# Kernel tuning notes

Measured on AMD Instinct MI355X. Metric: run time of the kernel, lower is better.

## Reference

```python
import jax, jax.numpy as jnp
import numpy as np

DIM = 64
B_GRAPHS = 16
N_NODES = 4096
N_EDGES = 16384
SLOPE = 0.01  # PyTorch leaky_relu default negative slope


def lrelu(x):
    return jnp.where(x >= 0, x, SLOPE * x)


def setup_inputs() -> dict:
    key = jax.random.key(0)
    ks = jax.random.split(key, 16)
    d = DIM

    def rn(k, shape, scale=0.05):
        return jax.random.normal(k, shape, dtype=jnp.float32) * scale

    def z(*s):
        return jnp.zeros(s, jnp.float32)

    return {
        "x": jax.random.normal(ks[0], (N_NODES, 3), dtype=jnp.float32),
        "edge_attr": jax.random.normal(ks[1], (N_EDGES, 4), dtype=jnp.float32),
        "edge_index": jax.random.randint(ks[2], (2, N_EDGES), 0, N_NODES),
        "batch": jnp.sort(jax.random.randint(ks[3], (N_NODES,), 0, B_GRAPHS)),
        # lin0
        "W0": rn(ks[4], (3, d)), "b0": z(d),
        # edge MLP: Linear(4,d) -> LeakyReLU -> Linear(d, d*d)
        "We1": rn(ks[5], (4, d)), "be1": z(d),
        "We2": rn(ks[6], (d, d * d), 0.01), "be2": z(d * d),
        # NNConv root weight + bias
        "root": rn(ks[7], (d, d)), "conv_b": z(d),
        # GRU(d, d)  (PyTorch layout: [3d, in] / [3d, hid], gate order r,z,n)
        "Wih": rn(ks[8], (3 * d, d)), "Whh": rn(ks[9], (3 * d, d)),
        "bih": z(3 * d), "bhh": z(3 * d),
        # Set2Set LSTM(2d, d)  (gate order i,f,g,o)
        "lWih": rn(ks[10], (4 * d, 2 * d)), "lWhh": rn(ks[11], (4 * d, d)),
        "lbih": z(4 * d), "lbhh": z(4 * d),
        # lin_out: Linear(2d, 2)
        "Wout": rn(ks[12], (2 * d, 2)), "bout": z(2),
    }


def _forward(x, edge_attr, W0, b0, We1, be1, We2, be2, root, conv_b,
             Wih, Whh, bih, bhh, lWih, lWhh, lbih, lbhh, Wout, bout,
             edge_index, batch):
    d = DIM
    N = x.shape[0]
    E = edge_attr.shape[0]
    src, dst = edge_index[0], edge_index[1]  # messages flow src(j) -> dst(i)

    out = lrelu(x @ W0 + b0)  # [N, d]
    h = out                    # GRU hidden state (h = out.unsqueeze(0))

    # Edge-conditioned weights: constant across the 6 iterations, compute once.
    he = lrelu(edge_attr @ We1 + be1)          # [E, d]
    W_e = (he @ We2 + be2).reshape(E, d, d)    # [E, d, d]
    deg = jax.ops.segment_sum(jnp.ones((E,), jnp.float32), dst, num_segments=N)
    inv_deg = (1.0 / jnp.maximum(deg, 1.0))[:, None]  # mean aggr, clamp like PyG

    for _ in range(6):
        # NNConv: gather x_j, per-edge matmul, scatter-mean, plus root term
        msg = jnp.einsum('ed,edf->ef', out[src], W_e)            # [E, d]
        agg = jax.ops.segment_sum(msg, dst, num_segments=N) * inv_deg
        m = lrelu(agg + out @ root + conv_b)                     # [N, d]
        # GRU cell (single step, PyTorch gate order r, z, n)
        gi = m @ Wih.T + bih
        gh = h @ Whh.T + bhh
        i_r, i_z, i_n = jnp.split(gi, 3, axis=-1)
        h_r, h_z, h_n = jnp.split(gh, 3, axis=-1)
        r = jax.nn.sigmoid(i_r + h_r)
        zg = jax.nn.sigmoid(i_z + h_z)
        n = jnp.tanh(i_n + r * h_n)
        h = (1.0 - zg) * n + zg * h
        out = h

    # Set2Set pooling, processing_steps = 1
    Bg = B_GRAPHS
    q_star = jnp.zeros((Bg, 2 * d), jnp.float32)
    hl = jnp.zeros((Bg, d), jnp.float32)
    cl = jnp.zeros((Bg, d), jnp.float32)
    gates = q_star @ lWih.T + lbih + hl @ lWhh.T + lbhh
    gi_, gf_, gg_, go_ = jnp.split(gates, 4, axis=-1)
    cl = jax.nn.sigmoid(gf_) * cl + jax.nn.sigmoid(gi_) * jnp.tanh(gg_)
    q = jax.nn.sigmoid(go_) * jnp.tanh(cl)         # [Bg, d]
    e = jnp.sum(out * q[batch], axis=-1)           # [N]
    emax = jax.ops.segment_max(e, batch, num_segments=Bg)
    a = jnp.exp(e - emax[batch])
    asum = jax.ops.segment_sum(a, batch, num_segments=Bg)
    a = a / asum[batch]                            # per-graph softmax attention
    rpool = jax.ops.segment_sum(a[:, None] * out, batch, num_segments=Bg)
    q_star = jnp.concatenate([q, rpool], axis=-1)  # [Bg, 2d]

    return q_star @ Wout + bout                    # [Bg, 2]


def reference(x, edge_attr, edge_index, batch, W0, b0, We1, be1, We2, be2,
              root, conv_b, Wih, Whh, bih, bhh, lWih, lWhh, lbih, lbhh,
              Wout, bout):
    return _forward(x, edge_attr, W0, b0, We1, be1, We2, be2, root, conv_b,
                    Wih, Whh, bih, bhh, lWih, lWhh, lbih, lbhh, Wout, bout,
                    edge_index, batch)
```

## Files before the change

### kernel.cpp

```cpp
#include <hip/hip_runtime.h>
#include <cstddef>

#define NE 16384
#define NN 4096
#define BG 16
#define NT 16
#define ACH 8

__device__ __forceinline__ float lrelu(float v){ return v >= 0.f ? v : 0.01f*v; }
__device__ __forceinline__ float sigm(float v){ return 1.f/(1.f + expf(-v)); }

__global__ __launch_bounds__(256) void setup_kernel(
    const float* __restrict__ x, const float* __restrict__ ea,
    const int* __restrict__ ei,
    const float* __restrict__ W0, const float* __restrict__ b0,
    const float* __restrict__ We1, const float* __restrict__ be1,
    const float* __restrict__ Wih, const float* __restrict__ Whh,
    float* __restrict__ W8T,
    float* __restrict__ h, float* __restrict__ he,
    int* __restrict__ deg, int* __restrict__ cnt)
{
    int t = blockIdx.x*256 + threadIdx.x;
    {
        int e = t >> 6, f = t & 63;
        float v = be1[f];
        #pragma unroll
        for (int d = 0; d < 4; ++d) v += ea[e*4+d]*We1[d*64+f];
        he[t] = lrelu(v);
    }
    if (t < NN*64) {
        int n = t >> 6, f = t & 63;
        float v = b0[f];
        #pragma unroll
        for (int d = 0; d < 3; ++d) v += x[n*3+d]*W0[d*64+f];
        h[t] = lrelu(v);
    }
    if (t < 32768) {
        int k = t >> 9, g = (t >> 3) & 63, j = t & 7;
        float v = 0.f;
        if (j < 3)      v = Wih[(j*64+g)*64 + k];
        else if (j < 6) v = Whh[((j-3)*64+g)*64 + k];
        W8T[t] = v;
    }
    if (t < NE) {
        atomicAdd(&deg[ei[NE + t]], 1);
        atomicAdd(&cnt[ei[t]], 1);
    }
}

__global__ __launch_bounds__(256) void scan_kernel(const int* __restrict__ cnt,
                                                   int* __restrict__ offs)
{
    __shared__ int ps[256];
    int t = threadIdx.x;
    int base = t*16;
    int loc[16];
    int s = 0;
    #pragma unroll
    for (int i = 0; i < 16; ++i) { loc[i] = s; s += cnt[base+i]; }
    ps[t] = s; __syncthreads();
    for (int off = 1; off < 256; off <<= 1) {
        int v = 0;
        if (t >= off) v = ps[t-off];
        __syncthreads();
        if (t >= off) ps[t] += v;
        __syncthreads();
    }
    int pre = (t == 0) ? 0 : ps[t-1];
    #pragma unroll
    for (int i = 0; i < 16; ++i) offs[base+i] = pre + loc[i];
    if (t == 255) offs[NN] = pre + s;
}

__global__ __launch_bounds__(256) void scatter_kernel(
    const int* __restrict__ ei, const int* __restrict__ offs,
    int* __restrict__ cnt,
    int* __restrict__ srcs, int* __restrict__ dsts, int* __restrict__ perm)
{
    int e = blockIdx.x*256 + threadIdx.x;
    if (e >= NE) return;
    int s = ei[e], d = ei[NE + e];
    int old = atomicSub(&cnt[s], 1);
    int pos = offs[s] + old - 1;
    srcs[pos] = s; dsts[pos] = d; perm[pos] = e;
}

__global__ __launch_bounds__(256) void reorder_kernel(
    const float* __restrict__ he, const int* __restrict__ perm,
    float* __restrict__ he_srt)
{
    int t = blockIdx.x*256 + threadIdx.x;
    he_srt[t] = he[(size_t)perm[t>>6]*64 + (t & 63)];
}

__global__ __launch_bounds__(256) void inv_range_kernel(
    const int* __restrict__ deg, const int* __restrict__ batch,
    float* __restrict__ inv_deg, int* __restrict__ gstart, int* __restrict__ gend)
{
    int n = blockIdx.x*256 + threadIdx.x;
    if (n >= NN) return;
    inv_deg[n] = 1.f / fmaxf((float)deg[n], 1.f);
    int b  = batch[n];
    int bp = (n == 0)    ? -1 : batch[n-1];
    int bn = (n == NN-1) ? BG : batch[n+1];
    for (int g = bp+1; g <= b; ++g) gstart[g] = n;
    for (int g = b;   g <  bn; ++g) gend[g]   = n+1;
    if (n == 0)    for (int g = 0;   g < b;  ++g) gend[g]   = 0;
    if (n == NN-1) for (int g = b+1; g < BG; ++g) gstart[g] = NN;
}

__global__ __launch_bounds__(1024) void conv_kernel(
    const float* __restrict__ h, const float* __restrict__ We2,
    const float* __restrict__ be2, const float* __restrict__ he_srt,
    const int* __restrict__ offs, const int* __restrict__ srcs,
    const int* __restrict__ dsts, float* __restrict__ agg)
{
    __shared__ float hsT[64][NT];
    __shared__ float Tb [NT][64];
    __shared__ float Tc [2][ACH][NT][64];
    __shared__ float he_s[2][128][ACH];
    int t  = threadIdx.x;
    int n0 = blockIdx.x * NT;

    { int n = t >> 6, i = t & 63; hsT[i][n] = h[(size_t)(n0+n)*64 + i]; }
    int ebase = offs[n0];
    int ecnt  = offs[n0+NT] - ebase;
    int eend  = ebase + ecnt;
    __syncthreads();

    int aT = t >> 6;
    int nT = ((t >> 4) & 3) * 4;
    int fT = (t & 15) * 4;
    int ct   = t - 512;
    int slot = ct >> 4;
    int f4   = (ct & 15) * 4;
    int nl0=-1,dt0=0,nl1=-1,dt1=0,nl2=-1,dt2=0,nl3=-1,dt3=0;
    float4 m0={0,0,0,0},m1={0,0,0,0},m2={0,0,0,0},m3={0,0,0,0};
    if (t >= 512) {
        if (slot      < ecnt) { nl0 = srcs[ebase+slot]    - n0; dt0 = dsts[ebase+slot];    }
        if (slot + 32 < ecnt) { nl1 = srcs[ebase+slot+32] - n0; dt1 = dsts[ebase+slot+32]; }
        if (slot + 64 < ecnt) { nl2 = srcs[ebase+slot+64] - n0; dt2 = dsts[ebase+slot+64]; }
        if (slot + 96 < ecnt) { nl3 = srcs[ebase+slot+96] - n0; dt3 = dsts[ebase+slot+96]; }
    }

#define EDGE_ACC(mj, nlj, row, buf_) \
    if (nlj >= 0) { \
        float4 hA = *(const float4*)&he_s[buf_][row][0]; \
        float4 hB = *(const float4*)&he_s[buf_][row][4]; \
        float4 t0 = *(const float4*)&Tc[buf_][0][nlj][f4]; \
        float4 t1 = *(const float4*)&Tc[buf_][1][nlj][f4]; \
        float4 t2 = *(const float4*)&Tc[buf_][2][nlj][f4]; \
        float4 t3 = *(const float4*)&Tc[buf_][3][nlj][f4]; \
        float4 t4 = *(const float4*)&Tc[buf_][4][nlj][f4]; \
        float4 t5 = *(const float4*)&Tc[buf_][5][nlj][f4]; \
        float4 t6 = *(const float4*)&Tc[buf_][6][nlj][f4]; \
        float4 t7 = *(const float4*)&Tc[buf_][7][nlj][f4]; \
        mj.x += hA.x*t0.x+hA.y*t1.x+hA.z*t2.x+hA.w*t3.x+hB.x*t4.x+hB.y*t5.x+hB.z*t6.x+hB.w*t7.x; \
        mj.y += hA.x*t0.y+hA.y*t1.y+hA.z*t2.y+hA.w*t3.y+hB.x*t4.y+hB.y*t5.y+hB.z*t6.y+hB.w*t7.y; \
        mj.z += hA.x*t0.z+hA.y*t1.z+hA.z*t2.z+hA.w*t3.z+hB.x*t4.z+hB.y*t5.z+hB.z*t6.z+hB.w*t7.z; \
        mj.w += hA.x*t0.w+hA.y*t1.w+hA.z*t2.w+hA.w*t3.w+hB.x*t4.w+hB.y*t5.w+hB.z*t6.w+hB.w*t7.w; \
    }

#define CONSUME(cm) { \
    int buf_ = (cm) & 1; \
    EDGE_ACC(m0, nl0, (slot),      buf_) \
    EDGE_ACC(m1, nl1, (slot+32),   buf_) \
    EDGE_ACC(m2, nl2, (slot+64),   buf_) \
    EDGE_ACC(m3, nl3, (slot+96),   buf_) \
    for (int e = ebase + 128 + slot; e < eend; e += 32) { \
        int nl = srcs[e] - n0, dtv = dsts[e]; \
        const float* hep = he_srt + (size_t)e*64 + (cm)*ACH; \
        float4 pm = {0,0,0,0}; \
        _Pragma("unroll") \
        for (int a = 0; a < ACH; ++a) { \
            float hv = hep[a]; \
            float4 tv = *(const float4*)&Tc[buf_][a][nl][f4]; \
            pm.x += hv*tv.x; pm.y += hv*tv.y; pm.z += hv*tv.z; pm.w += hv*tv.w; \
        } \
        if ((cm) == 0) { \
            float4 b = *(const float4*)&Tb[nl][f4]; \
            pm.x += b.x; pm.y += b.y; pm.z += b.z; pm.w += b.w; \
        } \
        float* ap = agg + (size_t)dtv*64 + f4; \
        atomicAdd(ap+0, pm.x); atomicAdd(ap+1, pm.y); \
        atomicAdd(ap+2, pm.z); atomicAdd(ap+3, pm.w); \
    } \
}

    for (int c = 0; c < 8; ++c) {
        if (t < 512) {
            const float* Wp = We2 + (size_t)(c*ACH + aT)*4096 + fT;
            float4 A0={0,0,0,0},A1={0,0,0,0},A2={0,0,0,0},A3={0,0,0,0};
            #pragma unroll 8
            for (int i = 0; i < 64; ++i) {
                float4 w  = *(const float4*)(Wp + (size_t)i*64);
                float4 hv = *(const float4*)&hsT[i][nT];
                A0.x += hv.x*w.x; A0.y += hv.x*w.y; A0.z += hv.x*w.z; A0.w += hv.x*w.w;
                A1.x += hv.y*w.x; A1.y += hv.y*w.y; A1.z += hv.y*w.z; A1.w += hv.y*w.w;
                A2.x += hv.z*w.x; A2.y += hv.z*w.y; A2.z += hv.z*w.z; A2.w += hv.z*w.w;
                A3.x += hv.w*w.x; A3.y += hv.w*w.y; A3.z += hv.w*w.z; A3.w += hv.w*w.w;
            }
            int buf = c & 1;
            *(float4*)&Tc[buf][aT][nT+0][fT] = A0;
            *(float4*)&Tc[buf][aT][nT+1][fT] = A1;
            *(float4*)&Tc[buf][aT][nT+2][fT] = A2;
            *(float4*)&Tc[buf][aT][nT+3][fT] = A3;
            if (c == 0) {
                #pragma unroll
                for (int r = 0; r < 2; ++r) {
                    int idx = t + r*512;
                    int n = idx >> 6, f = idx & 63;
                    float acc = 0.f;
                    #pragma unroll 8
                    for (int i = 0; i < 64; ++i) acc += hsT[i][n]*be2[i*64+f];
                    Tb[n][f] = acc;
                }
            }
        } else {
            {
                int le = ct >> 2, a2 = (ct & 3) * 2;
                if (ebase + le < NE)
                    *(float2*)&he_s[c&1][le][a2] =
                        *(const float2*)&he_srt[(size_t)(ebase+le)*64 + c*ACH + a2];
            }
            if (c >= 1) CONSUME(c-1);
        }
        __syncthreads();
    }
    if (t >= 512) {
        CONSUME(7);
        if (nl0 >= 0) {
            float4 b = *(const float4*)&Tb[nl0][f4];
            float* ap = agg + (size_t)dt0*64 + f4;
            atomicAdd(ap+0, m0.x+b.x); atomicAdd(ap+1, m0.y+b.y);
            atomicAdd(ap+2, m0.z+b.z); atomicAdd(ap+3, m0.w+b.w);
        }
        if (nl1 >= 0) {
            float4 b = *(const float4*)&Tb[nl1][f4];
            float* ap = agg + (size_t)dt1*64 + f4;
            atomicAdd(ap+0, m1.x+b.x); atomicAdd(ap+1, m1.y+b.y);
            atomicAdd(ap+2, m1.z+b.z); atomicAdd(ap+3, m1.w+b.w);
        }
        if (nl2 >= 0) {
            float4 b = *(const float4*)&Tb[nl2][f4];
            float* ap = agg + (size_t)dt2*64 + f4;
            atomicAdd(ap+0, m2.x+b.x); atomicAdd(ap+1, m2.y+b.y);
            atomicAdd(ap+2, m2.z+b.z); atomicAdd(ap+3, m2.w+b.w);
        }
        if (nl3 >= 0) {
            float4 b = *(const float4*)&Tb[nl3][f4];
            float* ap = agg + (size_t)dt3*64 + f4;
            atomicAdd(ap+0, m3.x+b.x); atomicAdd(ap+1, m3.y+b.y);
            atomicAdd(ap+2, m3.z+b.z); atomicAdd(ap+3, m3.w+b.w);
        }
    }
#undef CONSUME
#undef EDGE_ACC
}

__global__ __launch_bounds__(512) void node_kernel(
    const float* __restrict__ W8T, const float* __restrict__ root,
    const float* __restrict__ conv_b, const float* __restrict__ inv_deg,
    const float* __restrict__ bih, const float* __restrict__ bhh,
    float* __restrict__ h, float* __restrict__ agg)
{
    __shared__ float hs[8][64];
    __shared__ float ms[8][64];
    int t = threadIdx.x;
    int n = t >> 6, g = t & 63;
    int gn = blockIdx.x*8 + n;
    hs[n][g] = h[(size_t)gn*64 + g];
    __syncthreads();
    {
        size_t ix = (size_t)gn*64 + g;
        float v = agg[ix]*inv_deg[gn] + conv_b[g];
        agg[ix] = 0.f;
        #pragma unroll 8
        for (int k = 0; k < 64; ++k) v += hs[n][k]*root[k*64 + g];
        ms[n][g] = lrelu(v);
    }
    __syncthreads();

    float ir=0.f, iz=0.f, in_=0.f, hr=0.f, hz=0.f, hn=0.f;
    const float* Wp = W8T + (size_t)g*8;
    #pragma unroll 8
    for (int k = 0; k < 64; ++k) {
        float am = ms[n][k], ah = hs[n][k];
        float4 w0 = *(const float4*)(Wp + (size_t)k*512);
        float4 w1 = *(const float4*)(Wp + (size_t)k*512 + 4);
        ir  += am*w0.x; iz += am*w0.y; in_ += am*w0.z;
        hr  += ah*w0.w; hz += ah*w1.x; hn  += ah*w1.y;
    }
    float r  = sigm(ir + bih[g]      + hr + bhh[g]);
    float z  = sigm(iz + bih[64+g]   + hz + bhh[64+g]);
    float nn = tanhf(in_ + bih[128+g] + r*(hn + bhh[128+g]));
    h[(size_t)gn*64 + g] = (1.f - z)*nn + z*hs[n][g];
}

__device__ __forceinline__ float q_val(const float* lbih, const float* lbhh, int g)
{
    float gi = lbih[g]     + lbhh[g];
    float gg = lbih[128+g] + lbhh[128+g];
    float go = lbih[192+g] + lbhh[192+g];
    return sigm(go)*tanhf(sigm(gi)*tanhf(gg));
}

__global__ __launch_bounds__(256) void e_kernel(
    const float* __restrict__ h, const float* __restrict__ lbih,
    const float* __restrict__ lbhh, float* __restrict__ e)
{
    __shared__ float qs[64];
    int t = threadIdx.x;
    if (t < 64) qs[t] = q_val(lbih, lbhh, t);
    __syncthreads();
    int w = t >> 6, f = t & 63;
    int n = blockIdx.x*4 + w;
    float p = h[(size_t)n*64 + f]*qs[f];
    #pragma unroll
    for (int off = 32; off; off >>= 1) p += __shfl_xor(p, off);
    if (f == 0) e[n] = p;
}

__global__ __launch_bounds__(1024) void pool_kernel(
    const float* __restrict__ h, float* __restrict__ e,
    const int* __restrict__ gstart, const int* __restrict__ gend,
    const float* __restrict__ lbih, const float* __restrict__ lbhh,
    const float* __restrict__ Wout, const float* __restrict__ bout,
    float* __restrict__ out)
{
    __shared__ float red[1024];
    __shared__ float rp[64];
    __shared__ float sval;
    int g = blockIdx.x, t = threadIdx.x;
    int s = gstart[g], en = gend[g];

    float mx = -1e30f;
    for (int n = s+t; n < en; n += 1024) mx = fmaxf(mx, e[n]);
    red[t] = mx; __syncthreads();
    for (int st = 512; st; st >>= 1) { if (t < st) red[t] = fmaxf(red[t], red[t+st]); __syncthreads(); }
    if (t == 0) sval = red[0];
    __syncthreads();
    float lmx = sval;
    __syncthreads();

    float sm = 0.f;
    for (int n = s+t; n < en; n += 1024) { float a = expf(e[n]-lmx); e[n] = a; sm += a; }
    red[t] = sm; __syncthreads();
    for (int st = 512; st; st >>= 1) { if (t < st) red[t] += red[t+st]; __syncthreads(); }
    if (t == 0) sval = (red[0] > 0.f) ? 1.f/red[0] : 0.f;
    __syncthreads();
    float inv_asum = sval;
    __syncthreads();

    int w = t >> 6, f = t & 63;
    float racc = 0.f;
    for (int n = s+w; n < en; n += 16) racc += e[n]*h[(size_t)n*64 + f];
    red[t] = racc; __syncthreads();
    if (w == 0) {
        float a = 0.f;
        #pragma unroll
        for (int i = 0; i < 16; ++i) a += red[i*64 + f];
        rp[f] = a*inv_asum;
    }
    __syncthreads();

    if (t < 64) {
        float qv = q_val(lbih, lbhh, t);
        float p0 = qv*Wout[t*2]   + rp[t]*Wout[(64+t)*2];
        float p1 = qv*Wout[t*2+1] + rp[t]*Wout[(64+t)*2+1];
        #pragma unroll
        for (int off = 32; off; off >>= 1) { p0 += __shfl_xor(p0, off); p1 += __shfl_xor(p1, off); }
        if (t == 0) { out[g*2] = p0 + bout[0]; out[g*2+1] = p1 + bout[1]; }
    }
}

extern "C" void kernel_launch(void* const* d_in, const int* in_sizes, int n_in,
                              void* d_out, int out_size, void* d_ws, size_t ws_size,
                              hipStream_t stream)
{
    const float* x      = (const float*)d_in[0];
    const float* ea     = (const float*)d_in[1];
    const int*   ei     = (const int*)  d_in[2];
    const int*   batch  = (const int*)  d_in[3];
    const float* W0     = (const float*)d_in[4];
    const float* b0     = (const float*)d_in[5];
    const float* We1    = (const float*)d_in[6];
    const float* be1    = (const float*)d_in[7];
    const float* We2    = (const float*)d_in[8];
    const float* be2    = (const float*)d_in[9];
    const float* root   = (const float*)d_in[10];
    const float* conv_b = (const float*)d_in[11];
    const float* Wih    = (const float*)d_in[12];
    const float* Whh    = (const float*)d_in[13];
    const float* bih    = (const float*)d_in[14];
    const float* bhh    = (const float*)d_in[15];
    const float* lbih   = (const float*)d_in[18];
    const float* lbhh   = (const float*)d_in[19];
    const float* Wout   = (const float*)d_in[20];
    const float* bout   = (const float*)d_in[21];
    float* out = (float*)d_out;

    float* W = (float*)d_ws;
    size_t off = 0;
    float* h       = W + off; off += (size_t)NN*64;
    float* he      = W + off; off += (size_t)NE*64;
    float* he_srt  = W + off; off += (size_t)NE*64;
    float* agg     = W + off; off += (size_t)NN*64;
    float* W8T     = W + off; off += 32768;
    float* inv_deg = W + off; off += NN;
    float* e       = W + off; off += NN;
    int*   deg     = (int*)(W + off); off += NN;
    int*   cnt     = (int*)(W + off); off += NN;
    int*   offs    = (int*)(W + off); off += NN+1;
    int*   srcs    = (int*)(W + off); off += NE;
    int*   dsts    = (int*)(W + off); off += NE;
    int*   perm    = (int*)(W + off); off += NE;
    int*   gstart  = (int*)(W + off); off += BG;
    int*   gend    = (int*)(W + off); off += BG;

    hipMemsetAsync(deg, 0, 2*NN*sizeof(int), stream);
    hipMemsetAsync(agg, 0, (size_t)NN*64*sizeof(float), stream);
    setup_kernel<<<4096, 256, 0, stream>>>(x, ea, ei, W0, b0, We1, be1, Wih, Whh,
                                           W8T, h, he, deg, cnt);
    scan_kernel<<<1, 256, 0, stream>>>(cnt, offs);
    scatter_kernel<<<64, 256, 0, stream>>>(ei, offs, cnt, srcs, dsts, perm);
    reorder_kernel<<<4096, 256, 0, stream>>>(he, perm, he_srt);
    inv_range_kernel<<<16, 256, 0, stream>>>(deg, batch, inv_deg, gstart, gend);

    for (int it = 0; it < 6; ++it) {
        conv_kernel<<<NN/NT, 1024, 0, stream>>>(h, We2, be2, he_srt,
                                                offs, srcs, dsts, agg);
        node_kernel<<<NN/8, 512, 0, stream>>>(W8T, root, conv_b,
                                              inv_deg, bih, bhh, h, agg);
    }

    e_kernel<<<NN/4, 256, 0, stream>>>(h, lbih, lbhh, e);
    pool_kernel<<<BG, 1024, 0, stream>>>(h, e, gstart, gend, lbih, lbhh, Wout, bout, out);
}
```

Baseline: 558.0 us.

## Retile conv kernel to 2x8 register blocks, prefetch We2, move bias GEMV to consumer threads

The producer half of the conv kernel now computes a 2-node by 8-feature tile per thread instead of 4x4, stores h in a paired layout, and software-prefetches the next We2 rows to hide global load latency. The per-node bias term (h·be2) moves from producer threads at chunk 0 to the otherwise idle consumer threads. Consumer threads each handle 8 features and two resident edges instead of four features and four edges. The aim is fewer LDS reads per FMA and a shorter critical path for the producers, at the cost of higher register pressure and different atomic and edge-loop strides.

Result: slower. 830.6 us (+48.9%).

```diff
diff --git a/kernel.cpp b/kernel.cpp
--- a/kernel.cpp
+++ b/kernel.cpp
@@ -9,6 +9,9 @@
 
 __device__ __forceinline__ float lrelu(float v){ return v >= 0.f ? v : 0.01f*v; }
 __device__ __forceinline__ float sigm(float v){ return 1.f/(1.f + expf(-v)); }
+__device__ __forceinline__ void fma4(float4& a, float s, const float4& w){
+    a.x += s*w.x; a.y += s*w.y; a.z += s*w.z; a.w += s*w.w;
+}
 
 __global__ __launch_bounds__(256) void setup_kernel(
     const float* __restrict__ x, const float* __restrict__ ea,
@@ -115,107 +118,111 @@
     const int* __restrict__ offs, const int* __restrict__ srcs,
     const int* __restrict__ dsts, float* __restrict__ agg)
 {
-    __shared__ float hsT[64][NT];
+    __shared__ float hs2[32][16][2];
     __shared__ float Tb [NT][64];
     __shared__ float Tc [2][ACH][NT][64];
     __shared__ float he_s[2][128][ACH];
     int t  = threadIdx.x;
     int n0 = blockIdx.x * NT;
 
-    { int n = t >> 6, i = t & 63; hsT[i][n] = h[(size_t)(n0+n)*64 + i]; }
+    if (t < 512) {
+        int n = t & 15, r2 = t >> 4;
+        *(float2*)&hs2[r2][n][0] = *(const float2*)&h[(size_t)(n0+n)*64 + r2*2];
+    }
     int ebase = offs[n0];
     int ecnt  = offs[n0+NT] - ebase;
     int eend  = ebase + ecnt;
     __syncthreads();
 
-    int aT = t >> 6;
-    int nT = ((t >> 4) & 3) * 4;
-    int fT = (t & 15) * 4;
+    int aT  = t >> 6;
+    int nA  = ((t >> 3) & 7)*2;
+    int fT8 = (t & 7) * 8;
     int ct   = t - 512;
-    int slot = ct >> 4;
-    int f4   = (ct & 15) * 4;
-    int nl0=-1,dt0=0,nl1=-1,dt1=0,nl2=-1,dt2=0,nl3=-1,dt3=0;
-    float4 m0={0,0,0,0},m1={0,0,0,0},m2={0,0,0,0},m3={0,0,0,0};
+    int slot = ct >> 3;
+    int cf8  = (ct & 7) * 8;
+    int nl0=-1, dt0=0, nl1=-1, dt1=0;
+    float4 m0a={0,0,0,0}, m0b={0,0,0,0}, m1a={0,0,0,0}, m1b={0,0,0,0};
     if (t >= 512) {
         if (slot      < ecnt) { nl0 = srcs[ebase+slot]    - n0; dt0 = dsts[ebase+slot];    }
-        if (slot + 32 < ecnt) { nl1 = srcs[ebase+slot+32] - n0; dt1 = dsts[ebase+slot+32]; }
-        if (slot + 64 < ecnt) { nl2 = srcs[ebase+slot+64] - n0; dt2 = dsts[ebase+slot+64]; }
-        if (slot + 96 < ecnt) { nl3 = srcs[ebase+slot+96] - n0; dt3 = dsts[ebase+slot+96]; }
-    }
-
-#define EDGE_ACC(mj, nlj, row, buf_) \
+        if (slot + 64 < ecnt) { nl1 = srcs[ebase+slot+64] - n0; dt1 = dsts[ebase+slot+64]; }
+    }
+
+#define EDGE_ACC(mA, mB, nlj, row, buf_) \
     if (nlj >= 0) { \
         float4 hA = *(const float4*)&he_s[buf_][row][0]; \
         float4 hB = *(const float4*)&he_s[buf_][row][4]; \
-        float4 t0 = *(const float4*)&Tc[buf_][0][nlj][f4]; \
-        float4 t1 = *(const float4*)&Tc[buf_][1][nlj][f4]; \
-        float4 t2 = *(const float4*)&Tc[buf_][2][nlj][f4]; \
-        float4 t3 = *(const float4*)&Tc[buf_][3][nlj][f4]; \
-        float4 t4 = *(const float4*)&Tc[buf_][4][nlj][f4]; \
-        float4 t5 = *(const float4*)&Tc[buf_][5][nlj][f4]; \
-        float4 t6 = *(const float4*)&Tc[buf_][6][nlj][f4]; \
-        float4 t7 = *(const float4*)&Tc[buf_][7][nlj][f4]; \
-        mj.x += hA.x*t0.x+hA.y*t1.x+hA.z*t2.x+hA.w*t3.x+hB.x*t4.x+hB.y*t5.x+hB.z*t6.x+hB.w*t7.x; \
-        mj.y += hA.x*t0.y+hA.y*t1.y+hA.z*t2.y+hA.w*t3.y+hB.x*t4.y+hB.y*t5.y+hB.z*t6.y+hB.w*t7.y; \
-        mj.z += hA.x*t0.z+hA.y*t1.z+hA.z*t2.z+hA.w*t3.z+hB.x*t4.z+hB.y*t5.z+hB.z*t6.z+hB.w*t7.z; \
-        mj.w += hA.x*t0.w+hA.y*t1.w+hA.z*t2.w+hA.w*t3.w+hB.x*t4.w+hB.y*t5.w+hB.z*t6.w+hB.w*t7.w; \
+        float he8[8] = {hA.x,hA.y,hA.z,hA.w,hB.x,hB.y,hB.z,hB.w}; \
+        _Pragma("unroll") \
+        for (int a_ = 0; a_ < 8; ++a_) { \
+            float4 tA = *(const float4*)&Tc[buf_][a_][nlj][cf8]; \
+            float4 tB = *(const float4*)&Tc[buf_][a_][nlj][cf8+4]; \
+            fma4(mA, he8[a_], tA); \
+            fma4(mB, he8[a_], tB); \
+        } \
     }
 
 #define CONSUME(cm) { \
     int buf_ = (cm) & 1; \
-    EDGE_ACC(m0, nl0, (slot),      buf_) \
-    EDGE_ACC(m1, nl1, (slot+32),   buf_) \
-    EDGE_ACC(m2, nl2, (slot+64),   buf_) \
-    EDGE_ACC(m3, nl3, (slot+96),   buf_) \
-    for (int e = ebase + 128 + slot; e < eend; e += 32) { \
+    EDGE_ACC(m0a, m0b, nl0, slot,      buf_) \
+    EDGE_ACC(m1a, m1b, nl1, slot+64,   buf_) \
+    for (int e = ebase + 128 + slot; e < eend; e += 64) { \
         int nl = srcs[e] - n0, dtv = dsts[e]; \
         const float* hep = he_srt + (size_t)e*64 + (cm)*ACH; \
-        float4 pm = {0,0,0,0}; \
+        float4 pa = {0,0,0,0}, pb = {0,0,0,0}; \
         _Pragma("unroll") \
-        for (int a = 0; a < ACH; ++a) { \
-            float hv = hep[a]; \
-            float4 tv = *(const float4*)&Tc[buf_][a][nl][f4]; \
-            pm.x += hv*tv.x; pm.y += hv*tv.y; pm.z += hv*tv.z; pm.w += hv*tv.w; \
+        for (int a_ = 0; a_ < 8; ++a_) { \
+            float hv = hep[a_]; \
+            float4 tA = *(const float4*)&Tc[buf_][a_][nl][cf8]; \
+            float4 tB = *(const float4*)&Tc[buf_][a_][nl][cf8+4]; \
+            fma4(pa, hv, tA); \
+            fma4(pb, hv, tB); \
         } \
         if ((cm) == 0) { \
-            float4 b = *(const float4*)&Tb[nl][f4]; \
-            pm.x += b.x; pm.y += b.y; pm.z += b.z; pm.w += b.w; \
+            float4 bA = *(const float4*)&Tb[nl][cf8]; \
+            float4 bB = *(const float4*)&Tb[nl][cf8+4]; \
+            pa.x += bA.x; pa.y += bA.y; pa.z += bA.z; pa.w += bA.w; \
+            pb.x += bB.x; pb.y += bB.y; pb.z += bB.z; pb.w += bB.w; \
         } \
-        float* ap = agg + (size_t)dtv*64 + f4; \
-        atomicAdd(ap+0, pm.x); atomicAdd(ap+1, pm.y); \
-        atomicAdd(ap+2, pm.z); atomicAdd(ap+3, pm.w); \
+        float* ap = agg + (size_t)dtv*64 + cf8; \
+        atomicAdd(ap+0, pa.x); atomicAdd(ap+1, pa.y); \
+        atomicAdd(ap+2, pa.z); atomicAdd(ap+3, pa.w); \
+        atomicAdd(ap+4, pb.x); atomicAdd(ap+5, pb.y); \
+        atomicAdd(ap+6, pb.z); atomicAdd(ap+7, pb.w); \
     } \
 }
 
     for (int c = 0; c < 8; ++c) {
         if (t < 512) {
-            const float* Wp = We2 + (size_t)(c*ACH + aT)*4096 + fT;
-            float4 A0={0,0,0,0},A1={0,0,0,0},A2={0,0,0,0},A3={0,0,0,0};
-            #pragma unroll 8
-            for (int i = 0; i < 64; ++i) {
-                float4 w  = *(const float4*)(Wp + (size_t)i*64);
-                float4 hv = *(const float4*)&hsT[i][nT];
-                A0.x += hv.x*w.x; A0.y += hv.x*w.y; A0.z += hv.x*w.z; A0.w += hv.x*w.w;
-                A1.x += hv.y*w.x; A1.y += hv.y*w.y; A1.z += hv.y*w.z; A1.w += hv.y*w.w;
-                A2.x += hv.z*w.x; A2.y += hv.z*w.y; A2.z += hv.z*w.z; A2.w += hv.z*w.w;
-                A3.x += hv.w*w.x; A3.y += hv.w*w.y; A3.z += hv.w*w.z; A3.w += hv.w*w.w;
+            const float* Wp = We2 + (size_t)(c*ACH + aT)*4096 + fT8;
+            float4 a00={0,0,0,0}, a01={0,0,0,0}, a10={0,0,0,0}, a11={0,0,0,0};
+            float4 hv  = *(const float4*)&hs2[0][nA][0];
+            float4 wA0 = *(const float4*)(Wp);
+            float4 wA1 = *(const float4*)(Wp + 4);
+            float4 wB0 = *(const float4*)(Wp + 64);
+            float4 wB1 = *(const float4*)(Wp + 68);
+            #pragma unroll
+            for (int r2 = 0; r2 < 32; ++r2) {
+                float4 hvn={0,0,0,0}, wA0n={0,0,0,0}, wA1n={0,0,0,0},
+                       wB0n={0,0,0,0}, wB1n={0,0,0,0};
+                if (r2 < 31) {
+                    const float* Wn = Wp + (size_t)(r2+1)*128;
+                    hvn  = *(const float4*)&hs2[r2+1][nA][0];
+                    wA0n = *(const float4*)(Wn);
+                    wA1n = *(const float4*)(Wn + 4);
+                    wB0n = *(const float4*)(Wn + 64);
+                    wB1n = *(const float4*)(Wn + 68);
+                }
+                fma4(a00, hv.x, wA0); fma4(a01, hv.x, wA1);
+                fma4(a10, hv.z, wA0); fma4(a11, hv.z, wA1);
+                fma4(a00, hv.y, wB0); fma4(a01, hv.y, wB1);
+                fma4(a10, hv.w, wB0); fma4(a11, hv.w, wB1);
+                hv = hvn; wA0 = wA0n; wA1 = wA1n; wB0 = wB0n; wB1 = wB1n;
             }
             int buf = c & 1;
-            *(float4*)&Tc[buf][aT][nT+0][fT] = A0;
-            *(float4*)&Tc[buf][aT][nT+1][fT] = A1;
-            *(float4*)&Tc[buf][aT][nT+2][fT] = A2;
-            *(float4*)&Tc[buf][aT][nT+3][fT] = A3;
-            if (c == 0) {
-                #pragma unroll
-                for (int r = 0; r < 2; ++r) {
-                    int idx = t + r*512;
-                    int n = idx >> 6, f = idx & 63;
-                    float acc = 0.f;
-                    #pragma unroll 8
-                    for (int i = 0; i < 64; ++i) acc += hsT[i][n]*be2[i*64+f];
-                    Tb[n][f] = acc;
-                }
-            }
+            *(float4*)&Tc[buf][aT][nA  ][fT8]   = a00;
+            *(float4*)&Tc[buf][aT][nA  ][fT8+4] = a01;
+            *(float4*)&Tc[buf][aT][nA+1][fT8]   = a10;
+            *(float4*)&Tc[buf][aT][nA+1][fT8+4] = a11;
         } else {
             {
                 int le = ct >> 2, a2 = (ct & 3) * 2;
@@ -223,35 +230,44 @@
                     *(float2*)&he_s[c&1][le][a2] =
                         *(const float2*)&he_srt[(size_t)(ebase+le)*64 + c*ACH + a2];
             }
-            if (c >= 1) CONSUME(c-1);
+            if (c == 0) {
+                int n = ct >> 5, fp = (ct & 31) * 2;
+                float t0 = 0.f, t1 = 0.f;
+                #pragma unroll 8
+                for (int r2 = 0; r2 < 32; ++r2) {
+                    float2 hv2 = *(const float2*)&hs2[r2][n][0];
+                    float2 bA  = *(const float2*)&be2[(size_t)(r2*2)*64 + fp];
+                    float2 bB  = *(const float2*)&be2[(size_t)(r2*2+1)*64 + fp];
+                    t0 += hv2.x*bA.x + hv2.y*bB.x;
+                    t1 += hv2.x*bA.y + hv2.y*bB.y;
+                }
+                Tb[n][fp]   = t0;
+                Tb[n][fp+1] = t1;
+            } else {
+                CONSUME(c-1);
+            }
         }
         __syncthreads();
     }
     if (t >= 512) {
         CONSUME(7);
         if (nl0 >= 0) {
-            float4 b = *(const float4*)&Tb[nl0][f4];
-            float* ap = agg + (size_t)dt0*64 + f4;
-            atomicAdd(ap+0, m0.x+b.x); atomicAdd(ap+1, m0.y+b.y);
-            atomicAdd(ap+2, m0.z+b.z); atomicAdd(ap+3, m0.w+b.w);
+            float4 bA = *(const float4*)&Tb[nl0][cf8];
+            float4 bB = *(const float4*)&Tb[nl0][cf8+4];
+            float* ap = agg + (size_t)dt0*64 + cf8;
+            atomicAdd(ap+0, m0a.x+bA.x); atomicAdd(ap+1, m0a.y+bA.y);
+            atomicAdd(ap+2, m0a.z+bA.z); atomicAdd(ap+3, m0a.w+bA.w);
+            atomicAdd(ap+4, m0b.x+bB.x); atomicAdd(ap+5, m0b.y+bB.y);
+            atomicAdd(ap+6, m0b.z+bB.z); atomicAdd(ap+7, m0b.w+bB.w);
         }
         if (nl1 >= 0) {
-            float4 b = *(const float4*)&Tb[nl1][f4];
-            float* ap = agg + (size_t)dt1*64 + f4;
-            atomicAdd(ap+0, m1.x+b.x); atomicAdd(ap+1, m1.y+b.y);
-            atomicAdd(ap+2, m1.z+b.z); atomicAdd(ap+3, m1.w+b.w);
-        }
-        if (nl2 >= 0) {
-            float4 b = *(const float4*)&Tb[nl2][f4];
-            float* ap = agg + (size_t)dt2*64 + f4;
-            atomicAdd(ap+0, m2.x+b.x); atomicAdd(ap+1, m2.y+b.y);
-            atomicAdd(ap+2, m2.z+b.z); atomicAdd(ap+3, m2.w+b.w);
-        }
-        if (nl3 >= 0) {
-            float4 b = *(const float4*)&Tb[nl3][f4];
-            float* ap = agg + (size_t)dt3*64 + f4;
-            atomicAdd(ap+0, m3.x+b.x); atomicAdd(ap+1, m3.y+b.y);
-            atomicAdd(ap+2, m3.z+b.z); atomicAdd(ap+3, m3.w+b.w);
+            float4 bA = *(const float4*)&Tb[nl1][cf8];
+            float4 bB = *(const float4*)&Tb[nl1][cf8+4];
+            float* ap = agg + (size_t)dt1*64 + cf8;
+            atomicAdd(ap+0, m1a.x+bA.x); atomicAdd(ap+1, m1a.y+bA.y);
+            atomicAdd(ap+2, m1a.z+bA.z); atomicAdd(ap+3, m1a.w+bA.w);
+            atomicAdd(ap+4, m1b.x+bB.x); atomicAdd(ap+5, m1b.y+bB.y);
+            atomicAdd(ap+6, m1b.z+bB.z); atomicAdd(ap+7, m1b.w+bB.w);
         }
     }
 #undef CONSUME
```

## Remap conv GEMM threads to node-rows and move bias product to consumer warps

Applied to the files above, without the earlier changes.

Each producer thread in the per-chunk h·We2 product now owns one node row and 16 contiguous output columns, keeping 32 h values in registers and streaming four float4 weight loads per input row. The h tile and Tc buffers are padded to 68 columns to reduce LDS bank conflicts. The c==0 bias projection Tb moves from the producer threads to the otherwise idle consumer threads, balancing work in the first iteration. This raises register pressure and changes global access patterns for We2, which could affect occupancy.

Result: slower. 1.833 ms (+228.5%).

```diff
diff --git a/kernel.cpp b/kernel.cpp
--- a/kernel.cpp
+++ b/kernel.cpp
@@ -9,6 +9,9 @@
 
 __device__ __forceinline__ float lrelu(float v){ return v >= 0.f ? v : 0.01f*v; }
 __device__ __forceinline__ float sigm(float v){ return 1.f/(1.f + expf(-v)); }
+__device__ __forceinline__ void fma4(float4& a, float s, const float4& w){
+    a.x += s*w.x; a.y += s*w.y; a.z += s*w.z; a.w += s*w.w;
+}
 
 __global__ __launch_bounds__(256) void setup_kernel(
     const float* __restrict__ x, const float* __restrict__ ea,
@@ -115,22 +118,25 @@
     const int* __restrict__ offs, const int* __restrict__ srcs,
     const int* __restrict__ dsts, float* __restrict__ agg)
 {
-    __shared__ float hsT[64][NT];
-    __shared__ float Tb [NT][64];
-    __shared__ float Tc [2][ACH][NT][64];
+    __shared__ float hs[NT][68];
+    __shared__ float Tb[NT][64];
+    __shared__ float Tc[2][ACH][NT][68];
     __shared__ float he_s[2][128][ACH];
     int t  = threadIdx.x;
     int n0 = blockIdx.x * NT;
 
-    { int n = t >> 6, i = t & 63; hsT[i][n] = h[(size_t)(n0+n)*64 + i]; }
+    if (t < 256) {
+        int n = t >> 4, j = (t & 15) * 4;
+        *(float4*)&hs[n][j] = *(const float4*)&h[(size_t)(n0+n)*64 + j];
+    }
     int ebase = offs[n0];
     int ecnt  = offs[n0+NT] - ebase;
     int eend  = ebase + ecnt;
     __syncthreads();
 
     int aT = t >> 6;
-    int nT = ((t >> 4) & 3) * 4;
-    int fT = (t & 15) * 4;
+    int nT = (t >> 2) & 15;
+    int fb = (t & 3) * 16;
     int ct   = t - 512;
     int slot = ct >> 4;
     int f4   = (ct & 15) * 4;
@@ -147,18 +153,12 @@
     if (nlj >= 0) { \
         float4 hA = *(const float4*)&he_s[buf_][row][0]; \
         float4 hB = *(const float4*)&he_s[buf_][row][4]; \
-        float4 t0 = *(const float4*)&Tc[buf_][0][nlj][f4]; \
-        float4 t1 = *(const float4*)&Tc[buf_][1][nlj][f4]; \
-        float4 t2 = *(const float4*)&Tc[buf_][2][nlj][f4]; \
-        float4 t3 = *(const float4*)&Tc[buf_][3][nlj][f4]; \
-        float4 t4 = *(const float4*)&Tc[buf_][4][nlj][f4]; \
-        float4 t5 = *(const float4*)&Tc[buf_][5][nlj][f4]; \
-        float4 t6 = *(const float4*)&Tc[buf_][6][nlj][f4]; \
-        float4 t7 = *(const float4*)&Tc[buf_][7][nlj][f4]; \
-        mj.x += hA.x*t0.x+hA.y*t1.x+hA.z*t2.x+hA.w*t3.x+hB.x*t4.x+hB.y*t5.x+hB.z*t6.x+hB.w*t7.x; \
-        mj.y += hA.x*t0.y+hA.y*t1.y+hA.z*t2.y+hA.w*t3.y+hB.x*t4.y+hB.y*t5.y+hB.z*t6.y+hB.w*t7.y; \
-        mj.z += hA.x*t0.z+hA.y*t1.z+hA.z*t2.z+hA.w*t3.z+hB.x*t4.z+hB.y*t5.z+hB.z*t6.z+hB.w*t7.z; \
-        mj.w += hA.x*t0.w+hA.y*t1.w+hA.z*t2.w+hA.w*t3.w+hB.x*t4.w+hB.y*t5.w+hB.z*t6.w+hB.w*t7.w; \
+        float he8[8] = {hA.x,hA.y,hA.z,hA.w,hB.x,hB.y,hB.z,hB.w}; \
+        _Pragma("unroll") \
+        for (int a_ = 0; a_ < 8; ++a_) { \
+            float4 tv = *(const float4*)&Tc[buf_][a_][nlj][f4]; \
+            fma4(mj, he8[a_], tv); \
+        } \
     }
 
 #define CONSUME(cm) { \
@@ -172,10 +172,10 @@
         const float* hep = he_srt + (size_t)e*64 + (cm)*ACH; \
         float4 pm = {0,0,0,0}; \
         _Pragma("unroll") \
-        for (int a = 0; a < ACH; ++a) { \
-            float hv = hep[a]; \
-            float4 tv = *(const float4*)&Tc[buf_][a][nl][f4]; \
-            pm.x += hv*tv.x; pm.y += hv*tv.y; pm.z += hv*tv.z; pm.w += hv*tv.w; \
+        for (int a_ = 0; a_ < 8; ++a_) { \
+            float hv = hep[a_]; \
+            float4 tv = *(const float4*)&Tc[buf_][a_][nl][f4]; \
+            fma4(pm, hv, tv); \
         } \
         if ((cm) == 0) { \
             float4 b = *(const float4*)&Tb[nl][f4]; \
@@ -189,41 +189,54 @@
 
     for (int c = 0; c < 8; ++c) {
         if (t < 512) {
-            const float* Wp = We2 + (size_t)(c*ACH + aT)*4096 + fT;
-            float4 A0={0,0,0,0},A1={0,0,0,0},A2={0,0,0,0},A3={0,0,0,0};
-            #pragma unroll 8
-            for (int i = 0; i < 64; ++i) {
-                float4 w  = *(const float4*)(Wp + (size_t)i*64);
-                float4 hv = *(const float4*)&hsT[i][nT];
-                A0.x += hv.x*w.x; A0.y += hv.x*w.y; A0.z += hv.x*w.z; A0.w += hv.x*w.w;
-                A1.x += hv.y*w.x; A1.y += hv.y*w.y; A1.z += hv.y*w.z; A1.w += hv.y*w.w;
-                A2.x += hv.z*w.x; A2.y += hv.z*w.y; A2.z += hv.z*w.z; A2.w += hv.z*w.w;
-                A3.x += hv.w*w.x; A3.y += hv.w*w.y; A3.z += hv.w*w.z; A3.w += hv.w*w.w;
+            const float* Wp = We2 + (size_t)(c*ACH + aT)*4096 + fb;
+            float4 a0={0,0,0,0}, a1={0,0,0,0}, a2={0,0,0,0}, a3={0,0,0,0};
+            #pragma unroll
+            for (int half = 0; half < 2; ++half) {
+                float hr[32];
+                #pragma unroll
+                for (int j = 0; j < 8; ++j) {
+                    float4 v = *(const float4*)&hs[nT][half*32 + j*4];
+                    hr[j*4]=v.x; hr[j*4+1]=v.y; hr[j*4+2]=v.z; hr[j*4+3]=v.w;
+                }
+                #pragma unroll
+                for (int i = 0; i < 32; ++i) {
+                    const float* wi = Wp + (size_t)(half*32 + i)*64;
+                    float4 w0 = *(const float4*)(wi);
+                    float4 w1 = *(const float4*)(wi + 4);
+                    float4 w2 = *(const float4*)(wi + 8);
+                    float4 w3 = *(const float4*)(wi + 12);
+                    float hv = hr[i];
+                    fma4(a0, hv, w0); fma4(a1, hv, w1);
+                    fma4(a2, hv, w2); fma4(a3, hv, w3);
+                }
             }
             int buf = c & 1;
-            *(float4*)&Tc[buf][aT][nT+0][fT] = A0;
-            *(float4*)&Tc[buf][aT][nT+1][fT] = A1;
-            *(float4*)&Tc[buf][aT][nT+2][fT] = A2;
-            *(float4*)&Tc[buf][aT][nT+3][fT] = A3;
-            if (c == 0) {
-                #pragma unroll
-                for (int r = 0; r < 2; ++r) {
-                    int idx = t + r*512;
-                    int n = idx >> 6, f = idx & 63;
-                    float acc = 0.f;
-                    #pragma unroll 8
-                    for (int i = 0; i < 64; ++i) acc += hsT[i][n]*be2[i*64+f];
-                    Tb[n][f] = acc;
-                }
-            }
+            *(float4*)&Tc[buf][aT][nT][fb]      = a0;
+            *(float4*)&Tc[buf][aT][nT][fb + 4]  = a1;
+            *(float4*)&Tc[buf][aT][nT][fb + 8]  = a2;
+            *(float4*)&Tc[buf][aT][nT][fb + 12] = a3;
         } else {
             {
-                int le = ct >> 2, a2 = (ct & 3) * 2;
+                int le = ct >> 2, a2s = (ct & 3) * 2;
                 if (ebase + le < NE)
-                    *(float2*)&he_s[c&1][le][a2] =
-                        *(const float2*)&he_srt[(size_t)(ebase+le)*64 + c*ACH + a2];
+                    *(float2*)&he_s[c&1][le][a2s] =
+                        *(const float2*)&he_srt[(size_t)(ebase+le)*64 + c*ACH + a2s];
             }
-            if (c >= 1) CONSUME(c-1);
+            if (c == 0) {
+                int n = ct >> 5, fp = (ct & 31) * 2;
+                float t0 = 0.f, t1 = 0.f;
+                #pragma unroll 8
+                for (int i = 0; i < 64; ++i) {
+                    float hv = hs[n][i];
+                    float2 b = *(const float2*)&be2[(size_t)i*64 + fp];
+                    t0 += hv*b.x; t1 += hv*b.y;
+                }
+                Tb[n][fp]   = t0;
+                Tb[n][fp+1] = t1;
+            } else {
+                CONSUME(c-1);
+            }
         }
         __syncthreads();
     }
```
